# Kernel optimization log

Measured on AMD Instinct MI355X. Metric: run time of the kernel, lower is better.

Reference implementation:

```python
import jax, jax.numpy as jnp
import numpy as np

N, F_IN, HID, EMB, HEADS, E = 20000, 256, 256, 128, 8, 160000
NEG_SLOPE = 0.2


def setup_inputs() -> dict:
    key = jax.random.key(0)
    ks = jax.random.split(key, 16)
    s = lambda fan: 1.0 / np.sqrt(fan)
    inp = {
        "x": jax.random.normal(ks[0], (N, F_IN), jnp.float32),
        "edge_index": jax.random.randint(ks[1], (2, E), 0, N, jnp.int64),
        "W1": jax.random.normal(ks[2], (F_IN, HID), jnp.float32) * s(F_IN),
        "b1": jnp.zeros((HID,), jnp.float32),
        "W2": jax.random.normal(ks[3], (HID, HID), jnp.float32) * s(HID),
        "b2": jnp.zeros((HID,), jnp.float32),
        "W3": jax.random.normal(ks[4], (HID, EMB), jnp.float32) * s(HID),
        "b3": jnp.zeros((EMB,), jnp.float32),
        "Wg": jax.random.normal(ks[5], (EMB, HEADS * EMB), jnp.float32) * s(EMB),
        "att_src": jax.random.normal(ks[6], (HEADS, EMB), jnp.float32) * s(EMB),
        "att_dst": jax.random.normal(ks[7], (HEADS, EMB), jnp.float32) * s(EMB),
        "bg": jnp.zeros((HEADS * EMB,), jnp.float32),
        "Wh1": jax.random.normal(ks[8], (HEADS * EMB, HID), jnp.float32) * s(HEADS * EMB),
        "bh1": jnp.zeros((HID,), jnp.float32),
        "Wh2": jax.random.normal(ks[9], (HID, 1), jnp.float32) * s(HID),
        "bh2": jnp.zeros((1,), jnp.float32),
    }
    return inp


def _gcn(x, W, b, src, dst, dinv):
    h = x @ W                                   # [N, out]
    msg = h[src] * (dinv[src] * dinv[dst])[:, None]  # gather + edge scale
    return jax.ops.segment_sum(msg, dst, N) + b


def _gat(x, Wg, att_src, att_dst, bg, src, dst):
    h = (x @ Wg).reshape(N, HEADS, EMB)          # [N, H, C]
    a_s = jnp.einsum('nhc,hc->nh', h, att_src)   # [N, H]
    a_d = jnp.einsum('nhc,hc->nh', h, att_dst)
    e = jax.nn.leaky_relu(a_s[src] + a_d[dst], NEG_SLOPE)  # [Etot, H]
    m = jax.ops.segment_max(e, dst, N)           # per-dst softmax max
    ex = jnp.exp(e - m[dst])
    denom = jax.ops.segment_sum(ex, dst, N)
    alpha = ex / denom[dst]                      # [Etot, H]
    out = jax.ops.segment_sum(h[src] * alpha[:, :, None], dst, N)
    return out.reshape(N, HEADS * EMB) + bg


def reference(x, edge_index, W1, b1, W2, b2, W3, b3, Wg, att_src, att_dst, bg, Wh1, bh1, Wh2, bh2):
    loops = jnp.arange(N, dtype=edge_index.dtype)
    src = jnp.concatenate([edge_index[0], loops])
    dst = jnp.concatenate([edge_index[1], loops])
    deg = jax.ops.segment_sum(jnp.ones_like(dst, dtype=x.dtype), dst, N)
    dinv = jax.lax.rsqrt(jnp.maximum(deg, 1.0))  # deg >= 1 due to self-loops

    h = jax.nn.relu(_gcn(x, W1, b1, src, dst, dinv))
    h = jax.nn.relu(_gcn(h, W2, b2, src, dst, dinv))
    h = jax.nn.relu(_gcn(h, W3, b3, src, dst, dinv))
    h = _gat(h, Wg, att_src, att_dst, bg, src, dst)
    z = jax.nn.relu(h @ Wh1 + bh1)
    logits = (z @ Wh2 + bh2).squeeze(-1)         # [N]
    w = jax.nn.sigmoid(logits)
    return jax.nn.softmax(w, axis=0)
```

## Files before the change

kernel.cpp:

```cpp
#include <hip/hip_runtime.h>
#include <math.h>

#define NN 20000
#define HEADS 8
#define M_PAD 20096

typedef _Float16 f16;
typedef f16 f16x2  __attribute__((ext_vector_type(2)));
typedef f16 f16x4v __attribute__((ext_vector_type(4)));
typedef f16 f16x8v __attribute__((ext_vector_type(8)));
typedef float f32x4 __attribute__((ext_vector_type(4)));

__device__ __forceinline__ float lrelu(float x){ return x > 0.f ? x : 0.2f*x; }

__global__ __launch_bounds__(256) void init_k(int* __restrict__ zbase, int zn,
        const float* __restrict__ W1, const float* __restrict__ W2, const float* __restrict__ W3,
        const float* __restrict__ Wg, const float* __restrict__ att_src, const float* __restrict__ att_dst,
        f16* __restrict__ wt1, f16* __restrict__ wt2, f16* __restrict__ wt3,
        f16* __restrict__ wasT)
{
    int t = blockIdx.x*256 + threadIdx.x;
    if (t < zn){ zbase[t] = 0; return; }
    t -= zn;
    if (t < 65536){ int k = t >> 8, n = t & 255; wt1[n*256 + k] = (f16)W1[t]; return; }
    t -= 65536;
    if (t < 65536){ int k = t >> 8, n = t & 255; wt2[n*256 + k] = (f16)W2[t]; return; }
    t -= 65536;
    if (t < 32768){ int k = t >> 7, n = t & 127; wt3[n*256 + k] = (f16)W3[t]; return; }
    t -= 32768;
    if (t < 8192){
        int r = t >> 7, k = t & 127;
        float s = 0.f;
        if (r < 16){
            const float* att = (r < 8) ? att_src : att_dst;
            int h = r & 7;
            const float* wg = Wg + (size_t)k*1024 + h*128;
            const float* at = att + h*128;
            for (int c = 0; c < 128; ++c) s = fmaf(wg[c], at[c], s);
        }
        wasT[r*128 + k] = (f16)s;
    }
}

__global__ __launch_bounds__(256) void wc_k(const float* __restrict__ Wg, const float* __restrict__ Wh1,
        const float* __restrict__ bg, const float* __restrict__ bh1,
        f16* __restrict__ wc_t, float* __restrict__ biasc)
{
    __shared__ float col[1024];
    __shared__ float red[256];
    const int j = blockIdx.x, t = threadIdx.x;
    float bsum = 0.f;
    #pragma unroll
    for (int i = 0; i < 4; ++i){
        int kk = i*256 + t;
        float v = Wh1[(size_t)kk*256 + j];
        col[kk] = v;
        bsum = fmaf(bg[kk], v, bsum);
    }
    red[t] = bsum; __syncthreads();
    for (int off = 128; off; off >>= 1){
        if (t < off) red[t] += red[t+off];
        __syncthreads();
    }
    if (!t) biasc[j] = red[0] + bh1[j];
    #pragma unroll
    for (int i = 0; i < 4; ++i){
        int k = i*256 + t;
        int h = k >> 7, kk = k & 127;
        const float* wg = Wg + (size_t)kk*1024 + h*128;
        const float* cl = col + h*128;
        float s = 0.f;
        for (int c = 0; c < 128; c += 4){
            float4 wv = *(const float4*)(wg + c);
            s = fmaf(wv.x, cl[c],   s);
            s = fmaf(wv.y, cl[c+1], s);
            s = fmaf(wv.z, cl[c+2], s);
            s = fmaf(wv.w, cl[c+3], s);
        }
        wc_t[(size_t)j*1024 + k] = (f16)s;
    }
}

__global__ __launch_bounds__(256) void hist_k(const int* __restrict__ dst, int* __restrict__ cnt, int E){
    int i = blockIdx.x*256 + threadIdx.x;
    if (i < E) atomicAdd(&cnt[dst[i]], 1);
}
__global__ __launch_bounds__(1024) void scan_k(const int* __restrict__ cnt, int* __restrict__ row_off,
                                               float* __restrict__ dinv){
    __shared__ int tot[1024];
    int t = threadIdx.x;
    const int CH = 20;
    int base = t*CH;
    int loc[CH]; int s = 0;
    #pragma unroll
    for (int i = 0; i < CH; ++i){
        int v = (base+i < NN) ? cnt[base+i] : 0;
        loc[i] = s; s += v;
    }
    tot[t] = s; __syncthreads();
    for (int off = 1; off < 1024; off <<= 1){
        int v = (t >= off) ? tot[t-off] : 0;
        __syncthreads();
        tot[t] += v;
        __syncthreads();
    }
    int pre = (t == 0) ? 0 : tot[t-1];
    #pragma unroll
    for (int i = 0; i < CH; ++i)
        if (base+i < NN){
            row_off[base+i] = pre + loc[i];
            dinv[base+i] = rsqrtf((float)cnt[base+i] + 1.f);
        }
    if (t == 1023) row_off[NN] = tot[1023];
}
__global__ __launch_bounds__(256) void scatter_k(const int* __restrict__ src, const int* __restrict__ dst,
        const int* __restrict__ row_off, int* __restrict__ cursor, int* __restrict__ src_sorted, int E){
    int i = blockIdx.x*256 + threadIdx.x;
    if (i >= E) return;
    int d = dst[i];
    int pos = row_off[d] + atomicAdd(&cursor[d], 1);
    src_sorted[pos] = src[i];
}

template<int EPI, int BN, bool A_F32, bool RELU, bool HAS_BIAS, int MINW>
__global__ __launch_bounds__(256, MINW) void gemm_f16_k(
        const void* __restrict__ Av, const f16* __restrict__ Bt,
        const float* __restrict__ bias, void* __restrict__ C,
        float* __restrict__ as_out, float* __restrict__ ad_out,
        const float* __restrict__ Wh2, float* __restrict__ logit,
        int M, int N, int K)
{
    constexpr int WN = BN/2;
    constexpr int NJ = WN/16;
    __shared__ __align__(16) f16 As[128*32];
    __shared__ __align__(16) f16 Bs[BN*32];
    const int tid  = threadIdx.x;
    const int lane = tid & 63;
    const int wave = tid >> 6;
    const int wm = (wave >> 1) * 64, wn = (wave & 1) * WN;
    const int l15 = lane & 15, quad = lane >> 4;
    const int m0 = blockIdx.y * 128, n0 = blockIdx.x * BN;

    const int r1 = tid >> 2;
    const int ce = (tid & 3) * 8;
    const int rowA0 = m0 + r1, rowA1 = rowA0 + 64;
    const f16*  Ah = (const f16*)Av;
    const float* Af = (const float*)Av;
    const f16* B0 = Bt + (size_t)(n0 + r1) * K + ce;
    const f16* B1 = B0 + (size_t)64 * K;

    f32x4 acc[4][NJ] = {};
    for (int k0 = 0; k0 < K; k0 += 32){
        if (A_F32){
            f16x8v h0 = {}, h1 = {};
            if (rowA0 < M){
                float4 p = *(const float4*)(Af + (size_t)rowA0*K + k0 + ce);
                float4 q = *(const float4*)(Af + (size_t)rowA0*K + k0 + ce + 4);
                h0[0]=(f16)p.x; h0[1]=(f16)p.y; h0[2]=(f16)p.z; h0[3]=(f16)p.w;
                h0[4]=(f16)q.x; h0[5]=(f16)q.y; h0[6]=(f16)q.z; h0[7]=(f16)q.w;
            }
            if (rowA1 < M){
                float4 p = *(const float4*)(Af + (size_t)rowA1*K + k0 + ce);
                float4 q = *(const float4*)(Af + (size_t)rowA1*K + k0 + ce + 4);
                h1[0]=(f16)p.x; h1[1]=(f16)p.y; h1[2]=(f16)p.z; h1[3]=(f16)p.w;
                h1[4]=(f16)q.x; h1[5]=(f16)q.y; h1[6]=(f16)q.z; h1[7]=(f16)q.w;
            }
            *(f16x8v*)&As[tid*8]        = h0;
            *(f16x8v*)&As[tid*8 + 2048] = h1;
        } else {
            *(uint4*)&As[tid*8]        = *(const uint4*)(Ah + (size_t)rowA0*K + k0 + ce);
            *(uint4*)&As[tid*8 + 2048] = *(const uint4*)(Ah + (size_t)rowA1*K + k0 + ce);
        }
        *(uint4*)&Bs[tid*8] = *(const uint4*)(B0 + k0);
        if (BN == 128)
            *(uint4*)&Bs[tid*8 + 2048] = *(const uint4*)(B1 + k0);
        __syncthreads();
        f16x8v af[4], bf[NJ];
        #pragma unroll
        for (int i = 0; i < 4; ++i)
            af[i] = *(const f16x8v*)&As[(wm + i*16 + l15)*32 + quad*8];
        #pragma unroll
        for (int j = 0; j < NJ; ++j)
            bf[j] = *(const f16x8v*)&Bs[(wn + j*16 + l15)*32 + quad*8];
        #pragma unroll
        for (int i = 0; i < 4; ++i)
            #pragma unroll
            for (int j = 0; j < NJ; ++j)
                acc[i][j] = __builtin_amdgcn_mfma_f32_16x16x32_f16(af[i], bf[j], acc[i][j], 0, 0, 0);
        __syncthreads();
    }

    if (EPI == 2){
        float b4[NJ], w4[NJ];
        #pragma unroll
        for (int j = 0; j < NJ; ++j){
            int cg = n0 + wn + j*16 + l15;
            b4[j] = bias[cg]; w4[j] = Wh2[cg];
        }
        #pragma unroll
        for (int i = 0; i < 4; ++i)
            #pragma unroll
            for (int r = 0; r < 4; ++r){
                float ps = 0.f;
                #pragma unroll
                for (int j = 0; j < NJ; ++j){
                    float v = fmaxf(acc[i][j][r] + b4[j], 0.f);
                    ps = fmaf(v, w4[j], ps);
                }
                ps += __shfl_xor(ps, 1, 64); ps += __shfl_xor(ps, 2, 64);
                ps += __shfl_xor(ps, 4, 64); ps += __shfl_xor(ps, 8, 64);
                if (l15 == 0){
                    int row = m0 + wm + i*16 + quad*4 + r;
                    if (row < M) unsafeAtomicAdd(&logit[row], ps);
                }
            }
        return;
    }

    if (EPI == 3){
        #pragma unroll
        for (int i = 0; i < 4; ++i){
            int rb = m0 + wm + i*16 + quad*4;
            #pragma unroll
            for (int j = 0; j < NJ; ++j){
                int col = n0 + wn + j*16 + l15;
                if (col >= 16) continue;
                #pragma unroll
                for (int r = 0; r < 4; ++r){
                    int row = rb + r;
                    if (row >= M) continue;
                    float v = acc[i][j][r];
                    if (col < 8) as_out[row*8 + col] = v;
                    else         ad_out[row*8 + col - 8] = v;
                }
            }
        }
        return;
    }

    #pragma unroll
    for (int i = 0; i < 4; ++i){
        int rb = m0 + wm + i*16 + quad*4;
        #pragma unroll
        for (int j = 0; j < NJ; ++j){
            int col = n0 + wn + j*16 + l15;
            float bv = HAS_BIAS ? bias[col] : 0.f;
            #pragma unroll
            for (int r = 0; r < 4; ++r){
                int row = rb + r;
                if (row >= M) continue;
                float v = acc[i][j][r] + bv;
                if (RELU) v = fmaxf(v, 0.f);
                ((f16*)C)[(size_t)row*N + col] = (f16)v;
            }
        }
    }
}

template<int F>
__global__ __launch_bounds__(256) void gcn_agg_f16_k(const f16* __restrict__ h, const int* __restrict__ row_off,
        const int* __restrict__ srcs, const float* __restrict__ dinv, const float* __restrict__ bias,
        f16* __restrict__ out)
{
    int wv = (blockIdx.x*256 + threadIdx.x) >> 6;
    int lane = threadIdx.x & 63;
    if (wv >= NN) return;
    float di = dinv[wv];
    int p = row_off[wv], r1 = row_off[wv+1];
    if (F == 256){
        f16x4v v = *(const f16x4v*)(h + (size_t)wv*256 + lane*4);
        float c = di*di;
        float a0 = (float)v[0]*c, a1 = (float)v[1]*c, a2 = (float)v[2]*c, a3 = (float)v[3]*c;
        for (; p+4 <= r1; p += 4){
            int s0 = srcs[p], s1 = srcs[p+1], s2 = srcs[p+2], s3 = srcs[p+3];
            float c0 = dinv[s0]*di, c1 = dinv[s1]*di, c2 = dinv[s2]*di, c3 = dinv[s3]*di;
            f16x4v u0 = *(const f16x4v*)(h + (size_t)s0*256 + lane*4);
            f16x4v u1 = *(const f16x4v*)(h + (size_t)s1*256 + lane*4);
            f16x4v u2 = *(const f16x4v*)(h + (size_t)s2*256 + lane*4);
            f16x4v u3 = *(const f16x4v*)(h + (size_t)s3*256 + lane*4);
            a0 = fmaf((float)u3[0], c3, fmaf((float)u2[0], c2, fmaf((float)u1[0], c1, fmaf((float)u0[0], c0, a0))));
            a1 = fmaf((float)u3[1], c3, fmaf((float)u2[1], c2, fmaf((float)u1[1], c1, fmaf((float)u0[1], c0, a1))));
            a2 = fmaf((float)u3[2], c3, fmaf((float)u2[2], c2, fmaf((float)u1[2], c1, fmaf((float)u0[2], c0, a2))));
            a3 = fmaf((float)u3[3], c3, fmaf((float)u2[3], c2, fmaf((float)u1[3], c1, fmaf((float)u0[3], c0, a3))));
        }
        for (; p < r1; ++p){
            int s0 = srcs[p];
            float c0 = dinv[s0]*di;
            f16x4v u0 = *(const f16x4v*)(h + (size_t)s0*256 + lane*4);
            a0 = fmaf((float)u0[0], c0, a0); a1 = fmaf((float)u0[1], c0, a1);
            a2 = fmaf((float)u0[2], c0, a2); a3 = fmaf((float)u0[3], c0, a3);
        }
        float4 bv = *(const float4*)(bias + lane*4);
        f16x4v o;
        o[0] = (f16)fmaxf(a0 + bv.x, 0.f); o[1] = (f16)fmaxf(a1 + bv.y, 0.f);
        o[2] = (f16)fmaxf(a2 + bv.z, 0.f); o[3] = (f16)fmaxf(a3 + bv.w, 0.f);
        *(f16x4v*)(out + (size_t)wv*256 + lane*4) = o;
    } else {
        f16x2 v = *(const f16x2*)(h + (size_t)wv*128 + lane*2);
        float c = di*di;
        float a0 = (float)v[0]*c, a1 = (float)v[1]*c;
        for (; p+4 <= r1; p += 4){
            int s0 = srcs[p], s1 = srcs[p+1], s2 = srcs[p+2], s3 = srcs[p+3];
            float c0 = dinv[s0]*di, c1 = dinv[s1]*di, c2 = dinv[s2]*di, c3 = dinv[s3]*di;
            f16x2 u0 = *(const f16x2*)(h + (size_t)s0*128 + lane*2);
            f16x2 u1 = *(const f16x2*)(h + (size_t)s1*128 + lane*2);
            f16x2 u2 = *(const f16x2*)(h + (size_t)s2*128 + lane*2);
            f16x2 u3 = *(const f16x2*)(h + (size_t)s3*128 + lane*2);
            a0 = fmaf((float)u3[0], c3, fmaf((float)u2[0], c2, fmaf((float)u1[0], c1, fmaf((float)u0[0], c0, a0))));
            a1 = fmaf((float)u3[1], c3, fmaf((float)u2[1], c2, fmaf((float)u1[1], c1, fmaf((float)u0[1], c0, a1))));
        }
        for (; p < r1; ++p){
            int s0 = srcs[p];
            float c0 = dinv[s0]*di;
            f16x2 u0 = *(const f16x2*)(h + (size_t)s0*128 + lane*2);
            a0 = fmaf((float)u0[0], c0, a0); a1 = fmaf((float)u0[1], c0, a1);
        }
        float2 bv = *(const float2*)(bias + lane*2);
        f16x2 o;
        o[0] = (f16)fmaxf(a0 + bv.x, 0.f); o[1] = (f16)fmaxf(a1 + bv.y, 0.f);
        *(f16x2*)(out + (size_t)wv*128 + lane*2) = o;
    }
}

__global__ __launch_bounds__(256) void gat_soft_k(const int* __restrict__ row_off, const int* __restrict__ srcs,
        const float* __restrict__ a_s, const float* __restrict__ a_d,
        float* __restrict__ ex_sorted, float* __restrict__ alpha_self, float* __restrict__ inv_den)
{
    int t = blockIdx.x*256 + threadIdx.x;
    if (t >= NN*HEADS) return;
    int d = t >> 3, h = t & 7;
    float ad = a_d[t];
    float eself = lrelu(a_s[t] + ad);
    float m = eself;
    int r0 = row_off[d], r1 = row_off[d+1];
    for (int p = r0; p < r1; ++p){
        int s = srcs[p];
        m = fmaxf(m, lrelu(a_s[s*HEADS + h] + ad));
    }
    float den = expf(eself - m);
    for (int p = r0; p < r1; ++p){
        int s = srcs[p];
        float x = expf(lrelu(a_s[s*HEADS + h] + ad) - m);
        ex_sorted[(size_t)p*HEADS + h] = x;
        den += x;
    }
    float id = 1.f / den;
    alpha_self[t] = expf(eself - m) * id;
    inv_den[t]    = id;
}

__global__ __launch_bounds__(256) void agg_k(const f16* __restrict__ fG, const int* __restrict__ row_off,
        const int* __restrict__ srcs, const float* __restrict__ exs, const float* __restrict__ aself,
        const float* __restrict__ idn, f16* __restrict__ agg)
{
    int wv = (blockIdx.x*256 + threadIdx.x) >> 6;
    int lane = threadIdx.x & 63;
    if (wv >= NN) return;
    f16x2 v = *(const f16x2*)(fG + (size_t)wv*128 + lane*2);
    float v0 = (float)v[0], v1 = (float)v[1];
    float id[8], acc0[8], acc1[8];
    #pragma unroll
    for (int h = 0; h < 8; ++h){
        float as = aself[wv*8 + h];
        acc0[h] = v0*as; acc1[h] = v1*as;
        id[h] = idn[wv*8 + h];
    }
    int p = row_off[wv], r1 = row_off[wv+1];
    for (; p+2 <= r1; p += 2){
        int s0 = srcs[p], s1 = srcs[p+1];
        f16x2 u0 = *(const f16x2*)(fG + (size_t)s0*128 + lane*2);
        f16x2 u1 = *(const f16x2*)(fG + (size_t)s1*128 + lane*2);
        float4 ea = *(const float4*)(exs + (size_t)p*8);
        float4 eb = *(const float4*)(exs + (size_t)p*8 + 4);
        float4 fa = *(const float4*)(exs + (size_t)(p+1)*8);
        float4 fb = *(const float4*)(exs + (size_t)(p+1)*8 + 4);
        float u00=(float)u0[0], u01=(float)u0[1], u10=(float)u1[0], u11=(float)u1[1];
        float e0[8] = {ea.x,ea.y,ea.z,ea.w,eb.x,eb.y,eb.z,eb.w};
        float e1[8] = {fa.x,fa.y,fa.z,fa.w,fb.x,fb.y,fb.z,fb.w};
        #pragma unroll
        for (int h = 0; h < 8; ++h){
            float al0 = e0[h]*id[h], al1 = e1[h]*id[h];
            acc0[h] = fmaf(u10, al1, fmaf(u00, al0, acc0[h]));
            acc1[h] = fmaf(u11, al1, fmaf(u01, al0, acc1[h]));
        }
    }
    for (; p < r1; ++p){
        int s0 = srcs[p];
        f16x2 u0 = *(const f16x2*)(fG + (size_t)s0*128 + lane*2);
        float4 ea = *(const float4*)(exs + (size_t)p*8);
        float4 eb = *(const float4*)(exs + (size_t)p*8 + 4);
        float u00=(float)u0[0], u01=(float)u0[1];
        float e0[8] = {ea.x,ea.y,ea.z,ea.w,eb.x,eb.y,eb.z,eb.w};
        #pragma unroll
        for (int h = 0; h < 8; ++h){
            float al0 = e0[h]*id[h];
            acc0[h] = fmaf(u00, al0, acc0[h]);
            acc1[h] = fmaf(u01, al0, acc1[h]);
        }
    }
    #pragma unroll
    for (int h = 0; h < 8; ++h){
        f16x2 o; o[0] = (f16)acc0[h]; o[1] = (f16)acc1[h];
        *(f16x2*)(agg + (size_t)wv*1024 + h*128 + lane*2) = o;
    }
}

__global__ __launch_bounds__(256) void head_sum_k(const float* __restrict__ logit, const float* __restrict__ bh2,
                                                  float* __restrict__ w, float* __restrict__ red){
    __shared__ float sm[256];
    int i = blockIdx.x*256 + threadIdx.x;
    float v = 0.f;
    if (i < NN){
        float s = 1.f / (1.f + expf(-(logit[i] + bh2[0])));
        w[i] = s;
        v = expf(s);
    }
    sm[threadIdx.x] = v; __syncthreads();
    for (int off = 128; off; off >>= 1){
        if (threadIdx.x < off) sm[threadIdx.x] += sm[threadIdx.x+off];
        __syncthreads();
    }
    if (!threadIdx.x) unsafeAtomicAdd(&red[0], sm[0]);
}
__global__ __launch_bounds__(256) void final_k(const float* __restrict__ w, const float* __restrict__ red,
                                               float* __restrict__ out){
    int i = blockIdx.x*256 + threadIdx.x;
    if (i >= NN) return;
    out[i] = expf(w[i]) / red[0];
}

extern "C" void kernel_launch(void* const* d_in, const int* in_sizes, int n_in,
                              void* d_out, int out_size, void* d_ws, size_t ws_size,
                              hipStream_t stream) {
    const float* x   = (const float*)d_in[0];
    const int*   ei  = (const int*)  d_in[1];
    const float* W1  = (const float*)d_in[2];
    const float* b1  = (const float*)d_in[3];
    const float* W2  = (const float*)d_in[4];
    const float* b2  = (const float*)d_in[5];
    const float* W3  = (const float*)d_in[6];
    const float* b3  = (const float*)d_in[7];
    const float* Wg  = (const float*)d_in[8];
    const float* att_src = (const float*)d_in[9];
    const float* att_dst = (const float*)d_in[10];
    const float* bg  = (const float*)d_in[11];
    const float* Wh1 = (const float*)d_in[12];
    const float* bh1 = (const float*)d_in[13];
    const float* Wh2 = (const float*)d_in[14];
    const float* bh2 = (const float*)d_in[15];
    float* out = (float*)d_out;

    const int E = in_sizes[1] / 2;
    const int* src = ei;
    const int* dst = ei + E;

    float* ws = (float*)d_ws;
    size_t o = 0;
    auto alloc = [&](size_t nfloats){ float* p = ws + o; o += (nfloats + 3) & ~(size_t)3; return p; };
    int* cnt    = (int*)alloc(NN);
    int* cursor = (int*)alloc(NN);
    float* logit= alloc(NN);
    float* red  = alloc(8);
    const int ZERO_N = 3*NN + 8;

    f16* wt1   = (f16*)alloc(65536/2);
    f16* wt2   = (f16*)alloc(65536/2);
    f16* wt3   = (f16*)alloc(32768/2);
    f16* wc_t  = (f16*)alloc(262144/2);
    f16* wasT  = (f16*)alloc(8192/2);
    float* biasc = alloc(256);
    f16* fH    = (f16*)alloc((size_t)M_PAD*256/2);
    f16* fG    = (f16*)alloc((size_t)M_PAD*256/2);
    f16* agg   = (f16*)alloc((size_t)M_PAD*1024/2);
    float* dinv = alloc(NN);
    float* a_s  = alloc((size_t)NN*HEADS);
    float* a_d  = alloc((size_t)NN*HEADS);
    float* aself= alloc((size_t)NN*HEADS);
    float* idn  = alloc((size_t)NN*HEADS);
    float* exs  = alloc((size_t)E*HEADS);
    float* wsig = alloc(NN);
    int* row_off= (int*)alloc(NN+1);
    int* src_srt= (int*)alloc(E);

    const int nb  = (NN + 255)/256;
    const int eb  = (E + 255)/256;
    const int nwb = (NN + 3)/4;
    const dim3 blk(256);
    const int MT = M_PAD/128;

    const int INIT_T = ZERO_N + 65536*2 + 32768 + 8192;
    init_k<<<(INIT_T + 255)/256, blk, 0, stream>>>(cnt, ZERO_N, W1, W2, W3, Wg, att_src, att_dst,
                                                   wt1, wt2, wt3, wasT);
    wc_k<<<256, blk, 0, stream>>>(Wg, Wh1, bg, bh1, wc_t, biasc);
    hist_k<<<eb, blk, 0, stream>>>(dst, cnt, E);
    scan_k<<<1, 1024, 0, stream>>>(cnt, row_off, dinv);
    scatter_k<<<eb, blk, 0, stream>>>(src, dst, row_off, cursor, src_srt, E);

    gemm_f16_k<0,64,true,false,false,4><<<dim3(4, MT), blk, 0, stream>>>(
        x, wt1, nullptr, fH, nullptr, nullptr, nullptr, nullptr, NN, 256, 256);
    gcn_agg_f16_k<256><<<nwb, blk, 0, stream>>>(fH, row_off, src_srt, dinv, b1, fG);
    gemm_f16_k<0,64,false,false,false,4><<<dim3(4, MT), blk, 0, stream>>>(
        fG, wt2, nullptr, fH, nullptr, nullptr, nullptr, nullptr, NN, 256, 256);
    gcn_agg_f16_k<256><<<nwb, blk, 0, stream>>>(fH, row_off, src_srt, dinv, b2, fG);
    gemm_f16_k<0,64,false,false,false,4><<<dim3(2, MT), blk, 0, stream>>>(
        fG, wt3, nullptr, fH, nullptr, nullptr, nullptr, nullptr, NN, 128, 256);
    gcn_agg_f16_k<128><<<nwb, blk, 0, stream>>>(fH, row_off, src_srt, dinv, b3, fG);

    gemm_f16_k<3,64,false,false,false,4><<<dim3(1, MT), blk, 0, stream>>>(
        fG, wasT, nullptr, nullptr, a_s, a_d, nullptr, nullptr, NN, 64, 128);
    gat_soft_k<<<(NN*HEADS)/256, blk, 0, stream>>>(row_off, src_srt, a_s, a_d, exs, aself, idn);
    agg_k<<<nwb, blk, 0, stream>>>(fG, row_off, src_srt, exs, aself, idn, agg);

    gemm_f16_k<2,64,false,true,true,4><<<dim3(4, MT), blk, 0, stream>>>(
        agg, wc_t, biasc, nullptr, nullptr, nullptr, Wh2, logit, NN, 256, 1024);

    head_sum_k<<<nb, blk, 0, stream>>>(logit, bh2, wsig, red);
    final_k<<<nb, blk, 0, stream>>>(wsig, red, out);
}
```

Measured before the change: 342.8 us.

## Fuse GAT softmax into aggregation and deepen GEMM K-tile with swizzled LDS

```diff
diff --git a/kernel.cpp b/kernel.cpp
--- a/kernel.cpp
+++ b/kernel.cpp
@@ -132,8 +132,8 @@
 {
     constexpr int WN = BN/2;
     constexpr int NJ = WN/16;
-    __shared__ __align__(16) f16 As[128*32];
-    __shared__ __align__(16) f16 Bs[BN*32];
+    __shared__ __align__(16) f16 As[128*64];
+    __shared__ __align__(16) f16 Bs[BN*64];
     const int tid  = threadIdx.x;
     const int lane = tid & 63;
     const int wave = tid >> 6;
@@ -141,52 +141,54 @@
     const int l15 = lane & 15, quad = lane >> 4;
     const int m0 = blockIdx.y * 128, n0 = blockIdx.x * BN;
 
-    const int r1 = tid >> 2;
-    const int ce = (tid & 3) * 8;
-    const int rowA0 = m0 + r1, rowA1 = rowA0 + 64;
+    const int rs = tid >> 3;
+    const int ce = (tid & 7) * 8;
+    const int swst = ((rs & 7) << 3);
+    const int swrd = ((l15 & 7) << 3);
     const f16*  Ah = (const f16*)Av;
     const float* Af = (const float*)Av;
-    const f16* B0 = Bt + (size_t)(n0 + r1) * K + ce;
-    const f16* B1 = B0 + (size_t)64 * K;
 
     f32x4 acc[4][NJ] = {};
-    for (int k0 = 0; k0 < K; k0 += 32){
-        if (A_F32){
-            f16x8v h0 = {}, h1 = {};
-            if (rowA0 < M){
-                float4 p = *(const float4*)(Af + (size_t)rowA0*K + k0 + ce);
-                float4 q = *(const float4*)(Af + (size_t)rowA0*K + k0 + ce + 4);
-                h0[0]=(f16)p.x; h0[1]=(f16)p.y; h0[2]=(f16)p.z; h0[3]=(f16)p.w;
-                h0[4]=(f16)q.x; h0[5]=(f16)q.y; h0[6]=(f16)q.z; h0[7]=(f16)q.w;
+    for (int k0 = 0; k0 < K; k0 += 64){
+        #pragma unroll
+        for (int pp = 0; pp < 4; ++pp){
+            int lr = rs + pp*32;
+            int grow = m0 + lr;
+            if (A_F32){
+                f16x8v hv = {};
+                if (grow < M){
+                    float4 p = *(const float4*)(Af + (size_t)grow*K + k0 + ce);
+                    float4 q = *(const float4*)(Af + (size_t)grow*K + k0 + ce + 4);
+                    hv[0]=(f16)p.x; hv[1]=(f16)p.y; hv[2]=(f16)p.z; hv[3]=(f16)p.w;
+                    hv[4]=(f16)q.x; hv[5]=(f16)q.y; hv[6]=(f16)q.z; hv[7]=(f16)q.w;
+                }
+                *(f16x8v*)&As[lr*64 + (ce ^ swst)] = hv;
+            } else {
+                *(uint4*)&As[lr*64 + (ce ^ swst)] = *(const uint4*)(Ah + (size_t)grow*K + k0 + ce);
             }
-            if (rowA1 < M){
-                float4 p = *(const float4*)(Af + (size_t)rowA1*K + k0 + ce);
-                float4 q = *(const float4*)(Af + (size_t)rowA1*K + k0 + ce + 4);
-                h1[0]=(f16)p.x; h1[1]=(f16)p.y; h1[2]=(f16)p.z; h1[3]=(f16)p.w;
-                h1[4]=(f16)q.x; h1[5]=(f16)q.y; h1[6]=(f16)q.z; h1[7]=(f16)q.w;
-            }
-            *(f16x8v*)&As[tid*8]        = h0;
-            *(f16x8v*)&As[tid*8 + 2048] = h1;
-        } else {
-            *(uint4*)&As[tid*8]        = *(const uint4*)(Ah + (size_t)rowA0*K + k0 + ce);
-            *(uint4*)&As[tid*8 + 2048] = *(const uint4*)(Ah + (size_t)rowA1*K + k0 + ce);
-        }
-        *(uint4*)&Bs[tid*8] = *(const uint4*)(B0 + k0);
-        if (BN == 128)
-            *(uint4*)&Bs[tid*8 + 2048] = *(const uint4*)(B1 + k0);
-        __syncthreads();
-        f16x8v af[4], bf[NJ];
-        #pragma unroll
-        for (int i = 0; i < 4; ++i)
-            af[i] = *(const f16x8v*)&As[(wm + i*16 + l15)*32 + quad*8];
-        #pragma unroll
-        for (int j = 0; j < NJ; ++j)
-            bf[j] = *(const f16x8v*)&Bs[(wn + j*16 + l15)*32 + quad*8];
-        #pragma unroll
-        for (int i = 0; i < 4; ++i)
+        }
+        #pragma unroll
+        for (int pp = 0; pp < BN/32; ++pp){
+            int lr = rs + pp*32;
+            *(uint4*)&Bs[lr*64 + (ce ^ swst)] = *(const uint4*)(Bt + (size_t)(n0 + lr)*K + k0 + ce);
+        }
+        __syncthreads();
+        #pragma unroll
+        for (int ks = 0; ks < 2; ++ks){
+            f16x8v af[4], bf[NJ];
+            const int rc = (ks*32 + quad*8) ^ swrd;
+            #pragma unroll
+            for (int i = 0; i < 4; ++i)
+                af[i] = *(const f16x8v*)&As[(wm + i*16 + l15)*64 + rc];
             #pragma unroll
             for (int j = 0; j < NJ; ++j)
-                acc[i][j] = __builtin_amdgcn_mfma_f32_16x16x32_f16(af[i], bf[j], acc[i][j], 0, 0, 0);
+                bf[j] = *(const f16x8v*)&Bs[(wn + j*16 + l15)*64 + rc];
+            #pragma unroll
+            for (int i = 0; i < 4; ++i)
+                #pragma unroll
+                for (int j = 0; j < NJ; ++j)
+                    acc[i][j] = __builtin_amdgcn_mfma_f32_16x16x32_f16(af[i], bf[j], acc[i][j], 0, 0, 0);
+        }
         __syncthreads();
     }
 
@@ -322,85 +324,60 @@
     }
 }
 
-__global__ __launch_bounds__(256) void gat_soft_k(const int* __restrict__ row_off, const int* __restrict__ srcs,
-        const float* __restrict__ a_s, const float* __restrict__ a_d,
-        float* __restrict__ ex_sorted, float* __restrict__ alpha_self, float* __restrict__ inv_den)
-{
-    int t = blockIdx.x*256 + threadIdx.x;
-    if (t >= NN*HEADS) return;
-    int d = t >> 3, h = t & 7;
-    float ad = a_d[t];
-    float eself = lrelu(a_s[t] + ad);
-    float m = eself;
-    int r0 = row_off[d], r1 = row_off[d+1];
-    for (int p = r0; p < r1; ++p){
-        int s = srcs[p];
-        m = fmaxf(m, lrelu(a_s[s*HEADS + h] + ad));
-    }
-    float den = expf(eself - m);
-    for (int p = r0; p < r1; ++p){
-        int s = srcs[p];
-        float x = expf(lrelu(a_s[s*HEADS + h] + ad) - m);
-        ex_sorted[(size_t)p*HEADS + h] = x;
-        den += x;
-    }
-    float id = 1.f / den;
-    alpha_self[t] = expf(eself - m) * id;
-    inv_den[t]    = id;
-}
-
-__global__ __launch_bounds__(256) void agg_k(const f16* __restrict__ fG, const int* __restrict__ row_off,
-        const int* __restrict__ srcs, const float* __restrict__ exs, const float* __restrict__ aself,
-        const float* __restrict__ idn, f16* __restrict__ agg)
+__global__ __launch_bounds__(256) void gatfuse_k(const f16* __restrict__ fG, const int* __restrict__ row_off,
+        const int* __restrict__ srcs, const float* __restrict__ a_s, const float* __restrict__ a_d,
+        f16* __restrict__ agg)
 {
     int wv = (blockIdx.x*256 + threadIdx.x) >> 6;
     int lane = threadIdx.x & 63;
     if (wv >= NN) return;
     f16x2 v = *(const f16x2*)(fG + (size_t)wv*128 + lane*2);
     float v0 = (float)v[0], v1 = (float)v[1];
-    float id[8], acc0[8], acc1[8];
+    float ad[8], es[8], m[8];
+    {
+        float4 s0 = *(const float4*)(a_s + (size_t)wv*8);
+        float4 s1 = *(const float4*)(a_s + (size_t)wv*8 + 4);
+        float4 d0 = *(const float4*)(a_d + (size_t)wv*8);
+        float4 d1 = *(const float4*)(a_d + (size_t)wv*8 + 4);
+        float asf[8] = {s0.x,s0.y,s0.z,s0.w,s1.x,s1.y,s1.z,s1.w};
+        float adf[8] = {d0.x,d0.y,d0.z,d0.w,d1.x,d1.y,d1.z,d1.w};
+        #pragma unroll
+        for (int h = 0; h < 8; ++h){ ad[h] = adf[h]; es[h] = lrelu(asf[h] + adf[h]); m[h] = es[h]; }
+    }
+    int r0 = row_off[wv], r1 = row_off[wv+1];
+    for (int p = r0; p < r1; ++p){
+        int s = srcs[p];
+        float4 s0 = *(const float4*)(a_s + (size_t)s*8);
+        float4 s1 = *(const float4*)(a_s + (size_t)s*8 + 4);
+        float e[8] = {s0.x,s0.y,s0.z,s0.w,s1.x,s1.y,s1.z,s1.w};
+        #pragma unroll
+        for (int h = 0; h < 8; ++h) m[h] = fmaxf(m[h], lrelu(e[h] + ad[h]));
+    }
+    float den[8], a0[8], a1[8];
     #pragma unroll
     for (int h = 0; h < 8; ++h){
-        float as = aself[wv*8 + h];
-        acc0[h] = v0*as; acc1[h] = v1*as;
-        id[h] = idn[wv*8 + h];
-    }
-    int p = row_off[wv], r1 = row_off[wv+1];
-    for (; p+2 <= r1; p += 2){
-        int s0 = srcs[p], s1 = srcs[p+1];
-        f16x2 u0 = *(const f16x2*)(fG + (size_t)s0*128 + lane*2);
-        f16x2 u1 = *(const f16x2*)(fG + (size_t)s1*128 + lane*2);
-        float4 ea = *(const float4*)(exs + (size_t)p*8);
-        float4 eb = *(const float4*)(exs + (size_t)p*8 + 4);
-        float4 fa = *(const float4*)(exs + (size_t)(p+1)*8);
-        float4 fb = *(const float4*)(exs + (size_t)(p+1)*8 + 4);
-        float u00=(float)u0[0], u01=(float)u0[1], u10=(float)u1[0], u11=(float)u1[1];
-        float e0[8] = {ea.x,ea.y,ea.z,ea.w,eb.x,eb.y,eb.z,eb.w};
-        float e1[8] = {fa.x,fa.y,fa.z,fa.w,fb.x,fb.y,fb.z,fb.w};
+        float w = expf(es[h] - m[h]);
+        den[h] = w; a0[h] = v0*w; a1[h] = v1*w;
+    }
+    for (int p = r0; p < r1; ++p){
+        int s = srcs[p];
+        float4 s0 = *(const float4*)(a_s + (size_t)s*8);
+        float4 s1 = *(const float4*)(a_s + (size_t)s*8 + 4);
+        f16x2 u = *(const f16x2*)(fG + (size_t)s*128 + lane*2);
+        float e[8] = {s0.x,s0.y,s0.z,s0.w,s1.x,s1.y,s1.z,s1.w};
+        float u0 = (float)u[0], u1 = (float)u[1];
         #pragma unroll
         for (int h = 0; h < 8; ++h){
-            float al0 = e0[h]*id[h], al1 = e1[h]*id[h];
-            acc0[h] = fmaf(u10, al1, fmaf(u00, al0, acc0[h]));
-            acc1[h] = fmaf(u11, al1, fmaf(u01, al0, acc1[h]));
-        }
-    }
-    for (; p < r1; ++p){
-        int s0 = srcs[p];
-        f16x2 u0 = *(const f16x2*)(fG + (size_t)s0*128 + lane*2);
-        float4 ea = *(const float4*)(exs + (size_t)p*8);
-        float4 eb = *(const float4*)(exs + (size_t)p*8 + 4);
-        float u00=(float)u0[0], u01=(float)u0[1];
-        float e0[8] = {ea.x,ea.y,ea.z,ea.w,eb.x,eb.y,eb.z,eb.w};
-        #pragma unroll
-        for (int h = 0; h < 8; ++h){
-            float al0 = e0[h]*id[h];
-            acc0[h] = fmaf(u00, al0, acc0[h]);
-            acc1[h] = fmaf(u01, al0, acc1[h]);
+            float w = expf(lrelu(e[h] + ad[h]) - m[h]);
+            den[h] += w;
+            a0[h] = fmaf(u0, w, a0[h]);
+            a1[h] = fmaf(u1, w, a1[h]);
         }
     }
     #pragma unroll
     for (int h = 0; h < 8; ++h){
-        f16x2 o; o[0] = (f16)acc0[h]; o[1] = (f16)acc1[h];
+        float inv = 1.f / den[h];
+        f16x2 o; o[0] = (f16)(a0[h]*inv); o[1] = (f16)(a1[h]*inv);
         *(f16x2*)(agg + (size_t)wv*1024 + h*128 + lane*2) = o;
     }
 }
@@ -475,9 +452,6 @@
     float* dinv = alloc(NN);
     float* a_s  = alloc((size_t)NN*HEADS);
     float* a_d  = alloc((size_t)NN*HEADS);
-    float* aself= alloc((size_t)NN*HEADS);
-    float* idn  = alloc((size_t)NN*HEADS);
-    float* exs  = alloc((size_t)E*HEADS);
     float* wsig = alloc(NN);
     int* row_off= (int*)alloc(NN+1);
     int* src_srt= (int*)alloc(E);
@@ -508,8 +482,7 @@
 
     gemm_f16_k<3,64,false,false,false,4><<<dim3(1, MT), blk, 0, stream>>>(
         fG, wasT, nullptr, nullptr, a_s, a_d, nullptr, nullptr, NN, 64, 128);
-    gat_soft_k<<<(NN*HEADS)/256, blk, 0, stream>>>(row_off, src_srt, a_s, a_d, exs, aself, idn);
-    agg_k<<<nwb, blk, 0, stream>>>(fG, row_off, src_srt, exs, aself, idn, agg);
+    gatfuse_k<<<nwb, blk, 0, stream>>>(fG, row_off, src_srt, a_s, a_d, agg);
 
     gemm_f16_k<2,64,false,true,true,4><<<dim3(4, MT), blk, 0, stream>>>(
         agg, wc_t, biasc, nullptr, nullptr, nullptr, Wh2, logit, NN, 256, 1024);
```

New measurement: 382.8 us. 1.12x slower.

## Deepen GEMM K-tile to 64 with XOR-swizzled LDS and use fast exp

Applied to the files above, without the earlier changes.

```diff
diff --git a/kernel.cpp b/kernel.cpp
--- a/kernel.cpp
+++ b/kernel.cpp
@@ -132,8 +132,8 @@
 {
     constexpr int WN = BN/2;
     constexpr int NJ = WN/16;
-    __shared__ __align__(16) f16 As[128*32];
-    __shared__ __align__(16) f16 Bs[BN*32];
+    __shared__ __align__(16) f16 As[128*64];
+    __shared__ __align__(16) f16 Bs[BN*64];
     const int tid  = threadIdx.x;
     const int lane = tid & 63;
     const int wave = tid >> 6;
@@ -141,52 +141,54 @@
     const int l15 = lane & 15, quad = lane >> 4;
     const int m0 = blockIdx.y * 128, n0 = blockIdx.x * BN;
 
-    const int r1 = tid >> 2;
-    const int ce = (tid & 3) * 8;
-    const int rowA0 = m0 + r1, rowA1 = rowA0 + 64;
+    const int rs = tid >> 3;
+    const int ce = (tid & 7) * 8;
+    const int swst = ((rs & 7) << 3);
+    const int swrd = ((l15 & 7) << 3);
     const f16*  Ah = (const f16*)Av;
     const float* Af = (const float*)Av;
-    const f16* B0 = Bt + (size_t)(n0 + r1) * K + ce;
-    const f16* B1 = B0 + (size_t)64 * K;
 
     f32x4 acc[4][NJ] = {};
-    for (int k0 = 0; k0 < K; k0 += 32){
-        if (A_F32){
-            f16x8v h0 = {}, h1 = {};
-            if (rowA0 < M){
-                float4 p = *(const float4*)(Af + (size_t)rowA0*K + k0 + ce);
-                float4 q = *(const float4*)(Af + (size_t)rowA0*K + k0 + ce + 4);
-                h0[0]=(f16)p.x; h0[1]=(f16)p.y; h0[2]=(f16)p.z; h0[3]=(f16)p.w;
-                h0[4]=(f16)q.x; h0[5]=(f16)q.y; h0[6]=(f16)q.z; h0[7]=(f16)q.w;
+    for (int k0 = 0; k0 < K; k0 += 64){
+        #pragma unroll
+        for (int pp = 0; pp < 4; ++pp){
+            int lr = rs + pp*32;
+            int grow = m0 + lr;
+            if (A_F32){
+                f16x8v hv = {};
+                if (grow < M){
+                    float4 p = *(const float4*)(Af + (size_t)grow*K + k0 + ce);
+                    float4 q = *(const float4*)(Af + (size_t)grow*K + k0 + ce + 4);
+                    hv[0]=(f16)p.x; hv[1]=(f16)p.y; hv[2]=(f16)p.z; hv[3]=(f16)p.w;
+                    hv[4]=(f16)q.x; hv[5]=(f16)q.y; hv[6]=(f16)q.z; hv[7]=(f16)q.w;
+                }
+                *(f16x8v*)&As[lr*64 + (ce ^ swst)] = hv;
+            } else {
+                *(uint4*)&As[lr*64 + (ce ^ swst)] = *(const uint4*)(Ah + (size_t)grow*K + k0 + ce);
             }
-            if (rowA1 < M){
-                float4 p = *(const float4*)(Af + (size_t)rowA1*K + k0 + ce);
-                float4 q = *(const float4*)(Af + (size_t)rowA1*K + k0 + ce + 4);
-                h1[0]=(f16)p.x; h1[1]=(f16)p.y; h1[2]=(f16)p.z; h1[3]=(f16)p.w;
-                h1[4]=(f16)q.x; h1[5]=(f16)q.y; h1[6]=(f16)q.z; h1[7]=(f16)q.w;
-            }
-            *(f16x8v*)&As[tid*8]        = h0;
-            *(f16x8v*)&As[tid*8 + 2048] = h1;
-        } else {
-            *(uint4*)&As[tid*8]        = *(const uint4*)(Ah + (size_t)rowA0*K + k0 + ce);
-            *(uint4*)&As[tid*8 + 2048] = *(const uint4*)(Ah + (size_t)rowA1*K + k0 + ce);
-        }
-        *(uint4*)&Bs[tid*8] = *(const uint4*)(B0 + k0);
-        if (BN == 128)
-            *(uint4*)&Bs[tid*8 + 2048] = *(const uint4*)(B1 + k0);
+        }
+        #pragma unroll
+        for (int pp = 0; pp < BN/32; ++pp){
+            int lr = rs + pp*32;
+            *(uint4*)&Bs[lr*64 + (ce ^ swst)] = *(const uint4*)(Bt + (size_t)(n0 + lr)*K + k0 + ce);
+        }
         __syncthreads();
-        f16x8v af[4], bf[NJ];
-        #pragma unroll
-        for (int i = 0; i < 4; ++i)
-            af[i] = *(const f16x8v*)&As[(wm + i*16 + l15)*32 + quad*8];
-        #pragma unroll
-        for (int j = 0; j < NJ; ++j)
-            bf[j] = *(const f16x8v*)&Bs[(wn + j*16 + l15)*32 + quad*8];
-        #pragma unroll
-        for (int i = 0; i < 4; ++i)
+        #pragma unroll
+        for (int ks = 0; ks < 2; ++ks){
+            f16x8v af[4], bf[NJ];
+            const int rc = (ks*32 + quad*8) ^ swrd;
+            #pragma unroll
+            for (int i = 0; i < 4; ++i)
+                af[i] = *(const f16x8v*)&As[(wm + i*16 + l15)*64 + rc];
             #pragma unroll
             for (int j = 0; j < NJ; ++j)
-                acc[i][j] = __builtin_amdgcn_mfma_f32_16x16x32_f16(af[i], bf[j], acc[i][j], 0, 0, 0);
+                bf[j] = *(const f16x8v*)&Bs[(wn + j*16 + l15)*64 + rc];
+            #pragma unroll
+            for (int i = 0; i < 4; ++i)
+                #pragma unroll
+                for (int j = 0; j < NJ; ++j)
+                    acc[i][j] = __builtin_amdgcn_mfma_f32_16x16x32_f16(af[i], bf[j], acc[i][j], 0, 0, 0);
+        }
         __syncthreads();
     }
 
@@ -337,15 +339,15 @@
         int s = srcs[p];
         m = fmaxf(m, lrelu(a_s[s*HEADS + h] + ad));
     }
-    float den = expf(eself - m);
+    float den = __expf(eself - m);
     for (int p = r0; p < r1; ++p){
         int s = srcs[p];
-        float x = expf(lrelu(a_s[s*HEADS + h] + ad) - m);
+        float x = __expf(lrelu(a_s[s*HEADS + h] + ad) - m);
         ex_sorted[(size_t)p*HEADS + h] = x;
         den += x;
     }
     float id = 1.f / den;
-    alpha_self[t] = expf(eself - m) * id;
+    alpha_self[t] = __expf(eself - m) * id;
     inv_den[t]    = id;
 }
 
```

Result: no change. 343.9 us (+0.3%).
